# Optimization experiments

Hardware: AMD Instinct MI355X
Metric: run time of the kernel (lower is better)

## Reference

```python
import jax, jax.numpy as jnp
import numpy as np

T = 15
L = 10.0
LAM = 0.1
RHO = 1.0
NUM_CONV_A = 32
NUM_CONV_B = 32
DICT_DIM = 7
STRIDE_A = 1
STRIDE_B = 1
DN = ('NCHW', 'OIHW', 'NCHW')


def _fro_normalize(W):
    # normalize each (d, d) filter slice by its Frobenius norm (torch F.normalize, p='fro', dim=(-1,-2))
    n = jnp.sqrt(jnp.sum(W * W, axis=(-1, -2), keepdims=True))
    return W / jnp.maximum(n, 1e-12)


def _conv(y, W, s):
    # torch F.conv2d(y, W, stride=s), VALID padding
    return jax.lax.conv_general_dilated(y, W, (s, s), 'VALID', dimension_numbers=DN)


def _convT(x, W, s):
    # torch F.conv_transpose2d(x, W, stride=s); W in forward-conv layout (O, I, kh, kw)
    return jax.lax.conv_transpose(x, W, (s, s), 'VALID', dimension_numbers=DN, transpose_kernel=True)


def setup_inputs() -> dict:
    key = jax.random.key(0)
    ky, ka, kb = jax.random.split(key, 3)
    y = jax.random.normal(ky, (16, 1, 256, 256), dtype=jnp.float32)
    A = _fro_normalize(jax.random.normal(ka, (NUM_CONV_A, 1, DICT_DIM, DICT_DIM), dtype=jnp.float32))
    B = _fro_normalize(jax.random.normal(kb, (NUM_CONV_B, 1, DICT_DIM, DICT_DIM), dtype=jnp.float32))
    return {'y': y, 'A': A, 'B': B}


def reference(y, A, B):
    n, _, H, W = y.shape
    Dx = (H - DICT_DIM) // STRIDE_A + 1
    Du = (H - DICT_DIM) // STRIDE_B + 1
    Dx2 = (W - DICT_DIM) // STRIDE_A + 1
    Du2 = (W - DICT_DIM) // STRIDE_B + 1
    x0 = jnp.zeros((n, NUM_CONV_A, Dx, Dx2), dtype=y.dtype)
    u0 = jnp.zeros((n, NUM_CONV_B, Du, Du2), dtype=y.dtype)

    def step(carry, _):
        x_old, x_tmp, u_old, u_tmp, t_old = carry
        Ax = _convT((1.0 + 1.0 / RHO) * x_tmp, A, STRIDE_A)
        Bu = _convT(u_tmp, B, STRIDE_B)
        res = y - (Ax + Bu)
        x_new = x_tmp + _conv(res, A, STRIDE_A) / L
        u_new = u_tmp + _conv(res, B, STRIDE_B) / L
        # twosided soft-threshold
        u_new = jax.nn.relu(jnp.abs(u_new) - LAM / L) * jnp.sign(u_new)
        t_new = (1.0 + jnp.sqrt(1.0 + 4.0 * t_old * t_old)) / 2.0
        c = (t_old - 1.0) / t_new
        x_tmp2 = x_new + c * (x_new - x_old)
        u_tmp2 = u_new + c * (u_new - u_old)
        return (x_new, x_tmp2, u_new, u_tmp2, t_new), None

    init = (x0, x0, u0, u0, jnp.float32(1.0))
    (x_new, _, u_new, _, _), _ = jax.lax.scan(step, init, None, length=T)

    Ax_hat = _convT(x_new, A, STRIDE_A)
    Bu_hat = _convT(u_new, B, STRIDE_B)
    y_hat = Ax_hat + Bu_hat
    return y_hat, x_new, u_new, Ax_hat, Bu_hat
```

## Files before the change

kernel.cpp:

```cpp
#include <hip/hip_runtime.h>
#include <cmath>

#define NB 16
#define CC 32
#define HH 256
#define WW 256
#define DD 250
#define ALPHA 2.0f
#define INVL 0.1f
#define THR 0.01f

#define IMG_SZ (HH*WW)
#define IMG_TOT (NB*IMG_SZ)
#define FLD_SZ (DD*DD)
#define FLD_TOT ((size_t)NB*CC*FLD_SZ)

#define SRS 264

__device__ __forceinline__ float rfl(float x) {
    return __int_as_float(__builtin_amdgcn_readfirstlane(__float_as_int(x)));
}
__device__ __forceinline__ float sthr(float v) {
    float a = fabsf(v) - THR; a = a > 0.f ? a : 0.f;
    return (v > 0.f) ? a : ((v < 0.f) ? -a : 0.f);
}

#define CONV_ROW(ACC, Aa) do { \
    _Pragma("unroll") \
    for (int b = 0; b < 7; ++b) { \
        const float wv = wt[Aa][b]; \
        ACC.x += wv*win[b+0]; ACC.y += wv*win[b+1]; \
        ACC.z += wv*win[b+2]; ACC.w += wv*win[b+3]; \
    } } while (0)

#define GATH_ROW(ACC, Aa) do { \
    _Pragma("unroll") \
    for (int b = 0; b < 7; ++b) { \
        const float wv = wt[Aa][b]; \
        ACC.x += wv*win[8-b+0]; ACC.y += wv*win[8-b+1]; \
        ACC.z += wv*win[8-b+2]; ACC.w += wv*win[8-b+3]; \
    } } while (0)

__global__ __launch_bounds__(512) void k_step(
    const float* __restrict__ rin,
    const float* sx_cur, const float* su_cur,
    float* sx_on, float* su_on,
    float* __restrict__ Ximg, float* __restrict__ Uimg,
    const float* __restrict__ Afil, const float* __restrict__ Bfil,
    float cmom, int first)
{
    __shared__ __align__(16) float resT[22*SRS];
    __shared__ __align__(16) float stile[2][16*SRS];

    const int p0  = blockIdx.x * 16;
    const int f   = blockIdx.y;
    const int n   = blockIdx.z;
    const int tid = threadIdx.x;
    const bool isx = (f == 0);

    {
        float4 z = make_float4(0.f,0.f,0.f,0.f);
        float4* sp = (float4*)&stile[0][0];
        for (int i = tid; i < 2*16*SRS/4; i += 512) sp[i] = z;
    }
    {
        const float* rb = rin + (size_t)n * IMG_SZ;
        for (int i = tid; i < 22*66; i += 512) {
            int r  = i / 66;
            int c4 = (i - r*66) << 2;
            int gr = p0 + r;
            float4 v = make_float4(0.f,0.f,0.f,0.f);
            if (gr < HH && c4 < WW) v = *(const float4*)(rb + gr*WW + c4);
            *(float4*)&resT[r*SRS + c4] = v;
        }
    }
    __syncthreads();

    const int rg  = tid >> 6;
    const int q4  = (tid & 63) << 2;
    const bool qok = (q4 <= 248);
    const int p_0 = p0 + 2*rg;

    const float* Wb   = isx ? Afil : Bfil;
    const float* scur = isx ? sx_cur : su_cur;
    float*       sON  = isx ? sx_on  : su_on;
    float*       img  = (isx ? Ximg : Uimg) + (size_t)n * IMG_SZ;

    const bool momentum = (!first) && (cmom != 0.f);
    const bool plain    = (!first) && (cmom == 0.f);

    float4 ia0 = make_float4(0.f,0.f,0.f,0.f), ia1 = ia0, ia2 = ia0;

    const size_t fbase = (size_t)n * CC * FLD_SZ;
    const bool r0ok = qok && (p_0     < DD);
    const bool r1ok = qok && (p_0 + 1 < DD);
    const size_t off0 = fbase + (size_t)p_0*DD + q4;
    const size_t off1 = off0 + DD;

    for (int c = 0; c < CC; ++c) {
        float wt[7][7];
        {
            const float* Wp = Wb + c*49;
#pragma unroll
            for (int a = 0; a < 7; ++a)
#pragma unroll
                for (int b = 0; b < 7; ++b)
                    wt[a][b] = rfl(Wp[a*7 + b]);
        }

        const size_t co = (size_t)c * FLD_SZ;
        float4 sc0 = make_float4(0.f,0.f,0.f,0.f), sc1 = sc0, so0 = sc0, so1 = sc0;
        if (momentum) {
            if (r0ok) { sc0 = *(const float4*)(scur + co + off0);
                        so0 = *(const float4*)(sON  + co + off0); }
            if (r1ok) { sc1 = *(const float4*)(scur + co + off1);
                        so1 = *(const float4*)(sON  + co + off1); }
        } else if (plain) {
            if (r0ok) sc0 = *(const float4*)(scur + co + off0);
            if (r1ok) sc1 = *(const float4*)(scur + co + off1);
        }

        float4 a0 = make_float4(0.f,0.f,0.f,0.f), a1 = a0;
#pragma unroll
        for (int rr = 0; rr < 8; ++rr) {
            const float* lp = &resT[(2*rg + rr)*SRS + q4];
            float4 A0 = *(const float4*)lp;
            float4 A1 = *(const float4*)(lp + 4);
            float4 A2 = *(const float4*)(lp + 8);
            const float win[12] = {A0.x,A0.y,A0.z,A0.w, A1.x,A1.y,A1.z,A1.w,
                                   A2.x,A2.y,A2.z,A2.w};
            if (rr <= 6) CONV_ROW(a0, rr);
            if (rr >= 1) CONV_ROW(a1, rr-1);
        }

        float4 o0 = make_float4(a0.x*INVL, a0.y*INVL, a0.z*INVL, a0.w*INVL);
        float4 o1 = make_float4(a1.x*INVL, a1.y*INVL, a1.z*INVL, a1.w*INVL);
        if (momentum) {
            o0.x += sc0.x + cmom*(sc0.x - so0.x);
            o0.y += sc0.y + cmom*(sc0.y - so0.y);
            o0.z += sc0.z + cmom*(sc0.z - so0.z);
            o0.w += sc0.w + cmom*(sc0.w - so0.w);
            o1.x += sc1.x + cmom*(sc1.x - so1.x);
            o1.y += sc1.y + cmom*(sc1.y - so1.y);
            o1.z += sc1.z + cmom*(sc1.z - so1.z);
            o1.w += sc1.w + cmom*(sc1.w - so1.w);
        } else if (plain) {
            o0.x += sc0.x; o0.y += sc0.y; o0.z += sc0.z; o0.w += sc0.w;
            o1.x += sc1.x; o1.y += sc1.y; o1.z += sc1.z; o1.w += sc1.w;
        }
        if (!isx) {
            o0.x = sthr(o0.x); o0.y = sthr(o0.y); o0.z = sthr(o0.z); o0.w = sthr(o0.w);
            o1.x = sthr(o1.x); o1.y = sthr(o1.y); o1.z = sthr(o1.z); o1.w = sthr(o1.w);
        }

        if (r0ok) {
            float* dst = sON + co + off0;
            if (q4 <= 244) *(float4*)dst = o0;
            else           *(float2*)dst = make_float2(o0.x, o0.y);
        }
        if (r1ok) {
            float* dst = sON + co + off1;
            if (q4 <= 244) *(float4*)dst = o1;
            else           *(float2*)dst = make_float2(o1.x, o1.y);
        }

        const int bb = c & 1;
        if (r0ok) {
            float* d0 = &stile[bb][(2*rg)*SRS + q4 + 8];
            if (q4 <= 244) *(float4*)d0 = o0;
            else           *(float2*)d0 = make_float2(o0.x, o0.y);
        }
        if (r1ok) {
            float* d1 = &stile[bb][(2*rg + 1)*SRS + q4 + 8];
            if (q4 <= 244) *(float4*)d1 = o1;
            else           *(float2*)d1 = make_float2(o1.x, o1.y);
        }
        __syncthreads();

#pragma unroll
        for (int k9 = 0; k9 < 9; ++k9) {
            const int k = 3*rg - 6 + k9;
            if (k >= 0 && k < 16) {
                const float* sp = &stile[bb][k*SRS + q4];
                float4 B0 = *(const float4*)sp;
                float4 B1 = *(const float4*)(sp + 4);
                float4 B2 = *(const float4*)(sp + 8);
                const float win[12] = {B0.x,B0.y,B0.z,B0.w, B1.x,B1.y,B1.z,B1.w,
                                       B2.x,B2.y,B2.z,B2.w};
                if (k9 <= 6)            GATH_ROW(ia0, 6 - k9);
                if (k9 >= 1 && k9 <= 7) GATH_ROW(ia1, 7 - k9);
                if (k9 >= 2)            GATH_ROW(ia2, 8 - k9);
            }
        }
    }

#pragma unroll
    for (int d = 0; d < 3; ++d) {
        const int h = 3*rg + d;
        if (h < 22) {
            const int habs = p0 + h;
            if (habs < HH) {
                float4 v = (d == 0) ? ia0 : (d == 1) ? ia1 : ia2;
                float* ip = img + (size_t)habs*WW + q4;
                if (h >= 6 && h <= 15) {
                    *(float4*)ip = v;
                } else {
                    atomicAdd(ip + 0, v.x);
                    atomicAdd(ip + 1, v.y);
                    atomicAdd(ip + 2, v.z);
                    atomicAdd(ip + 3, v.w);
                }
            }
        }
    }
}

__global__ __launch_bounds__(256) void k_res(
    const float* __restrict__ y,
    float* Xp, float* Up,
    float* Xc, float* Uc,
    float* __restrict__ resb, float cm)
{
    int i = blockIdx.x*256 + threadIdx.x;
    if (i >= IMG_TOT/4) return;
    float4 xc = ((const float4*)Xp)[i];
    float4 uc = ((const float4*)Up)[i];
    float4 xo = make_float4(0.f,0.f,0.f,0.f), uo = xo;
    if (cm != 0.f) {
        xo = ((const float4*)Xc)[i];
        uo = ((const float4*)Uc)[i];
    }
    ((float4*)Xc)[i] = xc;
    ((float4*)Uc)[i] = uc;
    float4 z = make_float4(0.f,0.f,0.f,0.f);
    ((float4*)Xp)[i] = z;
    ((float4*)Up)[i] = z;
    float4 yv = ((const float4*)y)[i];
    const float cp = 1.f + cm;
    float4 r;
    r.x = yv.x - ALPHA*(cp*xc.x - cm*xo.x) - (cp*uc.x - cm*uo.x);
    r.y = yv.y - ALPHA*(cp*xc.y - cm*xo.y) - (cp*uc.y - cm*uo.y);
    r.z = yv.z - ALPHA*(cp*xc.z - cm*xo.z) - (cp*uc.z - cm*uo.z);
    r.w = yv.w - ALPHA*(cp*xc.w - cm*xo.w) - (cp*uc.w - cm*uo.w);
    ((float4*)resb)[i] = r;
}

__global__ __launch_bounds__(256) void k_zero2(float* a, float* b)
{
    int i = blockIdx.x*256 + threadIdx.x;
    if (i < IMG_TOT/4) {
        float4 z = make_float4(0.f,0.f,0.f,0.f);
        ((float4*)a)[i] = z;
        ((float4*)b)[i] = z;
    }
}

__global__ __launch_bounds__(256) void k_final(
    const float* __restrict__ axh, const float* __restrict__ buh,
    float* __restrict__ yhat)
{
    int i = blockIdx.x*256 + threadIdx.x;
    if (i < IMG_TOT/4) {
        float4 x = ((const float4*)axh)[i];
        float4 u = ((const float4*)buh)[i];
        float4 s;
        s.x = x.x + u.x; s.y = x.y + u.y; s.z = x.z + u.z; s.w = x.w + u.w;
        ((float4*)yhat)[i] = s;
    }
}

extern "C" void kernel_launch(void* const* d_in, const int* in_sizes, int n_in,
                              void* d_out, int out_size, void* d_ws, size_t ws_size,
                              hipStream_t stream) {
    const float* y = (const float*)d_in[0];
    const float* A = (const float*)d_in[1];
    const float* B = (const float*)d_in[2];

    float* out  = (float*)d_out;
    float* yhat = out;
    float* xout = out + IMG_TOT;
    float* uout = xout + FLD_TOT;
    float* axh  = uout + FLD_TOT;
    float* buh  = axh + IMG_TOT;

    float* ws   = (float*)d_ws;
    float* Px0  = ws;
    float* Pu0  = Px0 + FLD_TOT;
    float* Xc   = Pu0 + FLD_TOT;
    float* Uc   = Xc + IMG_TOT;

    float* Px[2] = {Px0, xout};
    float* Pu[2] = {Pu0, uout};
    float* res   = yhat;

    float cv[15];
    {
        float t = 1.0f;
        for (int k = 0; k < 15; ++k) {
            float tn = (1.0f + sqrtf(1.0f + 4.0f*t*t)) * 0.5f;
            cv[k] = (t - 1.0f) / tn;
            t = tn;
        }
    }

    dim3 blk512(512), blk256(256);
    dim3 gS(16, 2, NB);
    int  gE = (IMG_TOT/4 + 255)/256;

    k_zero2<<<gE, blk256, 0, stream>>>(axh, buh);

    k_step<<<gS, blk512, 0, stream>>>(y, Px[0], Pu[0], Px[1], Pu[1],
                                      axh, buh, A, B, 0.0f, 1);

    for (int t = 1; t < 15; ++t) {
        float cm = cv[t-1];
        k_res<<<gE, blk256, 0, stream>>>(y, axh, buh, Xc, Uc, res, cm);
        k_step<<<gS, blk512, 0, stream>>>(res, Px[t&1], Pu[t&1],
                                          Px[(t+1)&1], Pu[(t+1)&1],
                                          axh, buh, A, B, cm, 0);
    }

    k_final<<<gE, blk256, 0, stream>>>(axh, buh, yhat);
}
```

Before: 4.218 ms.

## Eliminate per-step x field storage via linear accumulation of residuals

The x update is linear with no thresholding, so the final x field is rewritten as a correlation of A with a weighted sum of residuals whose coefficients are precomputed on the host. The x image contribution is then tracked in image space through momentum recurrences on the increments. Per-step reads and writes of the large x field are dropped, and a single k_xfield pass writes the output at the end. The cost is extra image-sized buffers, more elementwise work in k_res, and possible floating-point drift from the reordered accumulation.

After: 4.358 ms. 3.3% more time.

```diff
diff --git a/kernel.cpp b/kernel.cpp
--- a/kernel.cpp
+++ b/kernel.cpp
@@ -16,6 +16,7 @@
 #define FLD_TOT ((size_t)NB*CC*FLD_SZ)
 
 #define SRS 264
+#define LRS 260
 
 __device__ __forceinline__ float rfl(float x) {
     return __int_as_float(__builtin_amdgcn_readfirstlane(__float_as_int(x)));
@@ -43,9 +44,8 @@
 
 __global__ __launch_bounds__(512) void k_step(
     const float* __restrict__ rin,
-    const float* sx_cur, const float* su_cur,
-    float* sx_on, float* su_on,
-    float* __restrict__ Ximg, float* __restrict__ Uimg,
+    const float* su_cur, float* su_on,
+    float* __restrict__ Xinc, float* __restrict__ Uacc,
     const float* __restrict__ Afil, const float* __restrict__ Bfil,
     float cmom, int first)
 {
@@ -81,13 +81,11 @@
     const bool qok = (q4 <= 248);
     const int p_0 = p0 + 2*rg;
 
-    const float* Wb   = isx ? Afil : Bfil;
-    const float* scur = isx ? sx_cur : su_cur;
-    float*       sON  = isx ? sx_on  : su_on;
-    float*       img  = (isx ? Ximg : Uimg) + (size_t)n * IMG_SZ;
-
-    const bool momentum = (!first) && (cmom != 0.f);
-    const bool plain    = (!first) && (cmom == 0.f);
+    const float* Wb = isx ? Afil : Bfil;
+    float* img = (isx ? Xinc : Uacc) + (size_t)n * IMG_SZ;
+
+    const bool momentum = (!isx) && (!first) && (cmom != 0.f);
+    const bool plain    = (!isx) && (!first) && (cmom == 0.f);
 
     float4 ia0 = make_float4(0.f,0.f,0.f,0.f), ia1 = ia0, ia2 = ia0;
 
@@ -111,13 +109,13 @@
         const size_t co = (size_t)c * FLD_SZ;
         float4 sc0 = make_float4(0.f,0.f,0.f,0.f), sc1 = sc0, so0 = sc0, so1 = sc0;
         if (momentum) {
-            if (r0ok) { sc0 = *(const float4*)(scur + co + off0);
-                        so0 = *(const float4*)(sON  + co + off0); }
-            if (r1ok) { sc1 = *(const float4*)(scur + co + off1);
-                        so1 = *(const float4*)(sON  + co + off1); }
+            if (r0ok) { sc0 = *(const float4*)(su_cur + co + off0);
+                        so0 = *(const float4*)(su_on  + co + off0); }
+            if (r1ok) { sc1 = *(const float4*)(su_cur + co + off1);
+                        so1 = *(const float4*)(su_on  + co + off1); }
         } else if (plain) {
-            if (r0ok) sc0 = *(const float4*)(scur + co + off0);
-            if (r1ok) sc1 = *(const float4*)(scur + co + off1);
+            if (r0ok) sc0 = *(const float4*)(su_cur + co + off0);
+            if (r1ok) sc1 = *(const float4*)(su_cur + co + off1);
         }
 
         float4 a0 = make_float4(0.f,0.f,0.f,0.f), a1 = a0;
@@ -153,30 +151,28 @@
             o1.x = sthr(o1.x); o1.y = sthr(o1.y); o1.z = sthr(o1.z); o1.w = sthr(o1.w);
         }
 
-        if (r0ok) {
-            float* dst = sON + co + off0;
-            if (q4 <= 244) *(float4*)dst = o0;
-            else           *(float2*)dst = make_float2(o0.x, o0.y);
-        }
-        if (r1ok) {
-            float* dst = sON + co + off1;
-            if (q4 <= 244) *(float4*)dst = o1;
-            else           *(float2*)dst = make_float2(o1.x, o1.y);
-        }
-
         const int bb = c & 1;
         if (r0ok) {
+            if (!isx) {
+                float* dst = su_on + co + off0;
+                if (q4 <= 244) *(float4*)dst = o0;
+                else           *(float2*)dst = make_float2(o0.x, o0.y);
+            }
             float* d0 = &stile[bb][(2*rg)*SRS + q4 + 8];
             if (q4 <= 244) *(float4*)d0 = o0;
             else           *(float2*)d0 = make_float2(o0.x, o0.y);
         }
         if (r1ok) {
+            if (!isx) {
+                float* dst = su_on + co + off1;
+                if (q4 <= 244) *(float4*)dst = o1;
+                else           *(float2*)dst = make_float2(o1.x, o1.y);
+            }
             float* d1 = &stile[bb][(2*rg + 1)*SRS + q4 + 8];
             if (q4 <= 244) *(float4*)d1 = o1;
             else           *(float2*)d1 = make_float2(o1.x, o1.y);
         }
         __syncthreads();
-
 #pragma unroll
         for (int k9 = 0; k9 < 9; ++k9) {
             const int k = 3*rg - 6 + k9;
@@ -217,56 +213,171 @@
 
 __global__ __launch_bounds__(256) void k_res(
     const float* __restrict__ y,
-    float* Xp, float* Up,
-    float* Xc, float* Uc,
-    float* __restrict__ resb, float cm)
+    float* Xinc, float* Uacc,
+    const float* __restrict__ XAv,
+    float* XBv,
+    float* Uc,
+    float* __restrict__ resb, float* __restrict__ Racc,
+    float cb, float cm, float alf)
 {
     int i = blockIdx.x*256 + threadIdx.x;
     if (i >= IMG_TOT/4) return;
-    float4 xc = ((const float4*)Xp)[i];
-    float4 uc = ((const float4*)Up)[i];
-    float4 xo = make_float4(0.f,0.f,0.f,0.f), uo = xo;
-    if (cm != 0.f) {
-        xo = ((const float4*)Xc)[i];
-        uo = ((const float4*)Uc)[i];
-    }
-    ((float4*)Xc)[i] = xc;
-    ((float4*)Uc)[i] = uc;
     float4 z = make_float4(0.f,0.f,0.f,0.f);
-    ((float4*)Xp)[i] = z;
-    ((float4*)Up)[i] = z;
+
+    float4 xi = ((const float4*)Xinc)[i];  ((float4*)Xinc)[i] = z;
+    float4 ua = ((const float4*)Uacc)[i];  ((float4*)Uacc)[i] = z;
+    float4 xa = ((const float4*)XAv)[i];
+
+    float4 xt;
+    if (cb != 0.f) {
+        float4 xb = ((const float4*)XBv)[i];
+        const float cbp = 1.f + cb;
+        xt.x = cbp*xa.x - cb*xb.x + xi.x;
+        xt.y = cbp*xa.y - cb*xb.y + xi.y;
+        xt.z = cbp*xa.z - cb*xb.z + xi.z;
+        xt.w = cbp*xa.w - cb*xb.w + xi.w;
+    } else {
+        xt.x = xa.x + xi.x; xt.y = xa.y + xi.y;
+        xt.z = xa.z + xi.z; xt.w = xa.w + xi.w;
+    }
+    ((float4*)XBv)[i] = xt;
+
+    float4 ucp = z;
+    if (cm != 0.f) ucp = ((const float4*)Uc)[i];
+    ((float4*)Uc)[i] = ua;
+
     float4 yv = ((const float4*)y)[i];
     const float cp = 1.f + cm;
     float4 r;
-    r.x = yv.x - ALPHA*(cp*xc.x - cm*xo.x) - (cp*uc.x - cm*uo.x);
-    r.y = yv.y - ALPHA*(cp*xc.y - cm*xo.y) - (cp*uc.y - cm*uo.y);
-    r.z = yv.z - ALPHA*(cp*xc.z - cm*xo.z) - (cp*uc.z - cm*uo.z);
-    r.w = yv.w - ALPHA*(cp*xc.w - cm*xo.w) - (cp*uc.w - cm*uo.w);
+    r.x = yv.x - ALPHA*(cp*xt.x - cm*xa.x) - (cp*ua.x - cm*ucp.x);
+    r.y = yv.y - ALPHA*(cp*xt.y - cm*xa.y) - (cp*ua.y - cm*ucp.y);
+    r.z = yv.z - ALPHA*(cp*xt.z - cm*xa.z) - (cp*ua.z - cm*ucp.z);
+    r.w = yv.w - ALPHA*(cp*xt.w - cm*xa.w) - (cp*ua.w - cm*ucp.w);
     ((float4*)resb)[i] = r;
-}
-
-__global__ __launch_bounds__(256) void k_zero2(float* a, float* b)
+
+    float4 ra = ((const float4*)Racc)[i];
+    ra.x += alf*r.x; ra.y += alf*r.y; ra.z += alf*r.z; ra.w += alf*r.w;
+    ((float4*)Racc)[i] = ra;
+}
+
+__global__ __launch_bounds__(256) void k_xfield(
+    const float* __restrict__ Racc, const float* __restrict__ yimg,
+    float* __restrict__ xout, const float* __restrict__ Afil, float alf0)
+{
+    __shared__ float lr[22*LRS + 8];
+
+    const int c   = blockIdx.x;
+    const int p0  = blockIdx.y * 16;
+    const int n   = blockIdx.z;
+    const int tid = threadIdx.x;
+
+    const float* rb = Racc + (size_t)n * IMG_SZ;
+    const float* yb = yimg + (size_t)n * IMG_SZ;
+#pragma unroll
+    for (int it = 0; it < 6; ++it) {
+        int idx = tid + it*256;
+        if (idx < 22*64) {
+            int r = idx >> 6, c4 = (idx & 63) << 2;
+            int gr = p0 + r;
+            float4 v = make_float4(0.f,0.f,0.f,0.f);
+            if (gr < HH) {
+                float4 a = *(const float4*)(rb + gr*WW + c4);
+                float4 b = *(const float4*)(yb + gr*WW + c4);
+                v.x = a.x + alf0*b.x; v.y = a.y + alf0*b.y;
+                v.z = a.z + alf0*b.z; v.w = a.w + alf0*b.w;
+            }
+            *(float4*)&lr[r*LRS + c4] = v;
+        }
+    }
+    if (tid < 8) lr[22*LRS + tid] = 0.f;
+
+    float wt[7][7];
+    {
+        const float* Wp = Afil + c*49;
+#pragma unroll
+        for (int a = 0; a < 7; ++a)
+#pragma unroll
+            for (int b = 0; b < 7; ++b)
+                wt[a][b] = rfl(Wp[a*7 + b]);
+    }
+    __syncthreads();
+
+    const int tq = tid & 63;
+    const int pg = tid >> 6;
+    const int q4 = tq << 2;
+
+    float acc4[4][4];
+#pragma unroll
+    for (int k = 0; k < 4; ++k)
+#pragma unroll
+        for (int j = 0; j < 4; ++j) acc4[k][j] = 0.f;
+
+#pragma unroll
+    for (int rr = 0; rr < 10; ++rr) {
+        const float* lp = &lr[(pg*4 + rr)*LRS + q4];
+        float4 A0 = *(const float4*)lp;
+        float4 A1 = *(const float4*)(lp + 4);
+        float4 A2 = *(const float4*)(lp + 8);
+        const float win[12] = {A0.x,A0.y,A0.z,A0.w, A1.x,A1.y,A1.z,A1.w,
+                               A2.x,A2.y,A2.z,A2.w};
+#pragma unroll
+        for (int k = 0; k < 4; ++k) {
+            const int a = rr - k;
+            if (a >= 0 && a < 7) {
+                float4 t = make_float4(acc4[k][0], acc4[k][1], acc4[k][2], acc4[k][3]);
+                CONV_ROW(t, a);
+                acc4[k][0] = t.x; acc4[k][1] = t.y; acc4[k][2] = t.z; acc4[k][3] = t.w;
+            }
+        }
+    }
+
+    const size_t base = ((size_t)n*CC + c) * FLD_SZ;
+#pragma unroll
+    for (int k = 0; k < 4; ++k) {
+        int p = p0 + pg*4 + k;
+        if (p < DD) {
+            size_t off = base + (size_t)p*DD + q4;
+            float4 o = make_float4(acc4[k][0]*INVL, acc4[k][1]*INVL,
+                                   acc4[k][2]*INVL, acc4[k][3]*INVL);
+            if (q4 <= 244)      *(float4*)(xout + off) = o;
+            else if (q4 == 248) *(float2*)(xout + off) = make_float2(o.x, o.y);
+        }
+    }
+}
+
+__global__ __launch_bounds__(256) void k_zero4(float* a, float* b, float* c, float* d)
 {
     int i = blockIdx.x*256 + threadIdx.x;
     if (i < IMG_TOT/4) {
         float4 z = make_float4(0.f,0.f,0.f,0.f);
         ((float4*)a)[i] = z;
         ((float4*)b)[i] = z;
-    }
-}
-
-__global__ __launch_bounds__(256) void k_final(
-    const float* __restrict__ axh, const float* __restrict__ buh,
-    float* __restrict__ yhat)
+        ((float4*)c)[i] = z;
+        ((float4*)d)[i] = z;
+    }
+}
+
+__global__ __launch_bounds__(256) void k_finale(
+    const float* __restrict__ Xinc, const float* __restrict__ Uacc,
+    const float* __restrict__ XA, const float* __restrict__ XB, float cb,
+    float* __restrict__ axh, float* __restrict__ buh, float* __restrict__ yhat)
 {
     int i = blockIdx.x*256 + threadIdx.x;
-    if (i < IMG_TOT/4) {
-        float4 x = ((const float4*)axh)[i];
-        float4 u = ((const float4*)buh)[i];
-        float4 s;
-        s.x = x.x + u.x; s.y = x.y + u.y; s.z = x.z + u.z; s.w = x.w + u.w;
-        ((float4*)yhat)[i] = s;
-    }
+    if (i >= IMG_TOT/4) return;
+    float4 xi = ((const float4*)Xinc)[i];
+    float4 xa = ((const float4*)XA)[i];
+    float4 xb = ((const float4*)XB)[i];
+    float4 u  = ((const float4*)Uacc)[i];
+    const float cbp = 1.f + cb;
+    float4 xt;
+    xt.x = cbp*xa.x - cb*xb.x + xi.x;
+    xt.y = cbp*xa.y - cb*xb.y + xi.y;
+    xt.z = cbp*xa.z - cb*xb.z + xi.z;
+    xt.w = cbp*xa.w - cb*xb.w + xi.w;
+    ((float4*)axh)[i] = xt;
+    ((float4*)buh)[i] = u;
+    float4 s = make_float4(xt.x+u.x, xt.y+u.y, xt.z+u.z, xt.w+u.w);
+    ((float4*)yhat)[i] = s;
 }
 
 extern "C" void kernel_launch(void* const* d_in, const int* in_sizes, int n_in,
@@ -284,13 +395,16 @@
     float* buh  = axh + IMG_TOT;
 
     float* ws   = (float*)d_ws;
-    float* Px0  = ws;
-    float* Pu0  = Px0 + FLD_TOT;
-    float* Xc   = Pu0 + FLD_TOT;
-    float* Uc   = Xc + IMG_TOT;
-
-    float* Px[2] = {Px0, xout};
+    float* Pu0  = ws;
+    float* XP0  = Pu0 + FLD_TOT;
+    float* XP1  = XP0 + IMG_TOT;
+    float* Uc   = XP1 + IMG_TOT;
+    float* Xinc = Uc + IMG_TOT;
+    float* Uacc = Xinc + IMG_TOT;
+    float* Racc = Uacc + IMG_TOT;
+
     float* Pu[2] = {Pu0, uout};
+    float* XP[2] = {XP0, XP1};
     float* res   = yhat;
 
     float cv[15];
@@ -302,23 +416,38 @@
             t = tn;
         }
     }
+    float alpha[15];
+    {
+        double bp[15] = {0}, bc[15] = {0}, bn[15];
+        bc[0] = 1.0;
+        for (int t = 1; t < 15; ++t) {
+            double cm = (double)cv[t-1];
+            for (int s = 0; s < 15; ++s) bn[s] = (1.0+cm)*bc[s] - cm*bp[s];
+            bn[t] += 1.0;
+            for (int s = 0; s < 15; ++s) { bp[s] = bc[s]; bc[s] = bn[s]; }
+        }
+        for (int s = 0; s < 15; ++s) alpha[s] = (float)bc[s];
+    }
 
     dim3 blk512(512), blk256(256);
     dim3 gS(16, 2, NB);
     int  gE = (IMG_TOT/4 + 255)/256;
 
-    k_zero2<<<gE, blk256, 0, stream>>>(axh, buh);
-
-    k_step<<<gS, blk512, 0, stream>>>(y, Px[0], Pu[0], Px[1], Pu[1],
-                                      axh, buh, A, B, 0.0f, 1);
+    k_zero4<<<gE, blk256, 0, stream>>>(XP0, Xinc, Uacc, Racc);
+
+    k_step<<<gS, blk512, 0, stream>>>(y, Pu[0], Pu[1], Xinc, Uacc, A, B, 0.0f, 1);
 
     for (int t = 1; t < 15; ++t) {
-        float cm = cv[t-1];
-        k_res<<<gE, blk256, 0, stream>>>(y, axh, buh, Xc, Uc, res, cm);
-        k_step<<<gS, blk512, 0, stream>>>(res, Px[t&1], Pu[t&1],
-                                          Px[(t+1)&1], Pu[(t+1)&1],
-                                          axh, buh, A, B, cm, 0);
-    }
-
-    k_final<<<gE, blk256, 0, stream>>>(axh, buh, yhat);
-}
+        const float cm = cv[t-1];
+        const float cb = (t >= 2) ? cv[t-2] : 0.0f;
+        k_res<<<gE, blk256, 0, stream>>>(y, Xinc, Uacc,
+                                         XP[(t-1)&1], XP[t&1], Uc,
+                                         res, Racc, cb, cm, alpha[t]);
+        k_step<<<gS, blk512, 0, stream>>>(res, Pu[t&1], Pu[(t+1)&1],
+                                          Xinc, Uacc, A, B, cm, 0);
+    }
+
+    k_xfield<<<dim3(CC, 16, NB), blk256, 0, stream>>>(Racc, y, xout, A, alpha[0]);
+    k_finale<<<gE, blk256, 0, stream>>>(Xinc, Uacc, XP[0], XP[1], cv[13],
+                                        axh, buh, yhat);
+}
```
